# Performance work log

Hardware: AMD Instinct MI355X
Metric: run time of the kernel (lower is better)

The kernel has to match this reference:

```python
import jax, jax.numpy as jnp
import numpy as np
import math

B, T, LM, LD, LP, D = 32, 40, 24, 32, 16, 256
VM, VD, VP = 4000, 6000, 2000
LTOT = LM + LD + LP + 1


def _sdpa(q, k, v, scale=None):
    # softmax(q k^T [*scale]) v, over the last two dims (works for rank-3 and rank-4)
    a = jnp.matmul(q, jnp.swapaxes(k, -1, -2))
    if scale is not None:
        a = a * scale
    a = jax.nn.softmax(a, axis=-1)
    return jnp.matmul(a, v)


def _pos_table():
    # HiTANet-style sinusoidal table with a zero pad row at index 0
    pos = np.arange(T, dtype=np.float32)[:, None]
    j = np.arange(D)[None, :]
    ang = pos / np.power(10000.0, 2.0 * (j // 2) / float(D))
    pe = np.where(j % 2 == 0, np.sin(ang), np.cos(ang)).astype(np.float32)
    return jnp.asarray(np.concatenate([np.zeros((1, D), np.float32), pe], axis=0))


def setup_inputs():
    key = jax.random.key(0)
    ks = jax.random.split(key, 24)
    u = lambda k, shape, b: jax.random.uniform(k, shape, jnp.float32, -b, b)
    inp = {
        "med_codes": jax.random.randint(ks[0], (B, T, LM), 0, VM),
        "diag_codes": jax.random.randint(ks[1], (B, T, LD), 0, VD),
        "proc_codes": jax.random.randint(ks[2], (B, T, LP), 0, VP),
        "med_mask_code": (jax.random.uniform(ks[3], (B, T, LM, 1)) < 0.8).astype(jnp.float32),
        "diag_mask_code": (jax.random.uniform(ks[4], (B, T, LD, 1)) < 0.8).astype(jnp.float32),
        "proc_mask_code": (jax.random.uniform(ks[5], (B, T, LP, 1)) < 0.8).astype(jnp.float32),
        "seq_time_step": jax.random.uniform(ks[6], (B, T), jnp.float32) * 2.0,
        "input_len": jax.random.randint(ks[7], (B,), 1, T + 1),
        "emb_med": jax.random.normal(ks[8], (VM, D), jnp.float32) * 0.02,
        "emb_diag": jax.random.normal(ks[9], (VD, D), jnp.float32) * 0.02,
        "emb_proc": jax.random.normal(ks[10], (VP, D), jnp.float32) * 0.02,
        "bias_med": u(ks[11], (D,), 1.0 / math.sqrt(VM)),
        "W_sel": u(ks[12], (64, 1), 1.0),
        "b_sel": u(ks[13], (64,), 1.0),
        "W_time": u(ks[14], (D, 64), 1.0 / math.sqrt(64.0)),
        "b_time": u(ks[15], (D,), 1.0 / math.sqrt(64.0)),
        "Wg_med": u(ks[16], (D, D), 1.0 / math.sqrt(float(D))),
        "bg_med": u(ks[17], (D,), 1.0 / math.sqrt(float(D))),
        "Wg_diag": u(ks[18], (D, D), 1.0 / math.sqrt(float(D))),
        "bg_diag": u(ks[19], (D,), 1.0 / math.sqrt(float(D))),
        "Wg_proc": u(ks[20], (D, D), 1.0 / math.sqrt(float(D))),
        "bg_proc": u(ks[21], (D,), 1.0 / math.sqrt(float(D))),
        "hidden_size": 256,
    }
    return inp


def reference(med_codes, diag_codes, proc_codes, med_mask_code, diag_mask_code,
              proc_mask_code, seq_time_step, input_len, emb_med, emb_diag, emb_proc,
              bias_med, W_sel, b_sel, W_time, b_time, Wg_med, bg_med, Wg_diag,
              bg_diag, Wg_proc, bg_proc, hidden_size):
    scale = 1.0 / math.sqrt(hidden_size + 1e-7)

    # time encoding: W2(1 - tanh((W1 t + b1)^2)) + b2  -> [B,T,1,D]
    t = seq_time_step[:, :, None]                       # [B,T,1]
    tf = 1.0 - jnp.tanh((t @ W_sel.T + b_sel) ** 2)     # [B,T,64]
    tf = tf @ W_time.T + b_time                         # [B,T,D]
    time_feature = tf[:, :, None, :]                    # [B,T,1,D]

    # positional encoding: positions 1..len, 0 (pad row) beyond len
    pe = _pos_table()
    ar = jnp.arange(T)[None, :]
    pos_idx = jnp.where(ar < input_len[:, None], ar + 1, 0)
    output_pos = pe[pos_idx]                            # [B,T,D]

    # masked embedding gathers [B,T,L,D]
    out_med = emb_med[med_codes] * med_mask_code
    out_diag = emb_diag[diag_codes] * diag_mask_code
    out_proc = emb_proc[proc_codes] * proc_mask_code

    # time-gated sigmoid modulation
    def gate(out, Wg, bg):
        g = _sdpa(time_feature, out, out, scale)        # [B,T,1,D]
        g = jax.nn.sigmoid(g @ Wg.T + bg)
        return g * out                                  # broadcast over L

    out_med = gate(out_med, Wg_med, bg_med)
    out_diag = gate(out_diag, Wg_diag, bg_diag)
    out_proc = gate(out_proc, Wg_proc, bg_proc)

    # per-modality self-attention over flattened T*L tokens
    def visit_att(out, L):
        x = out.reshape(B, T * L, D)
        x = _sdpa(x, x, x, scale)
        return x.reshape(B, T, L, D)

    out_med = visit_att(out_med, LM)
    out_diag = visit_att(out_diag, LD)
    out_proc = visit_att(out_proc, LP)

    # concat-fusion self-attention over all code types + time token [B,T,LTOT,D]
    merge = jnp.concatenate([out_med, out_diag, out_proc, time_feature], axis=2)
    merge = _sdpa(merge, merge, merge, scale)

    # med branch (predDiag=False, predProc=False): re-concat of the splits == merge
    out_med = merge[:, :, :LM]
    merge_aux = merge.reshape(B * T, LTOT, D)
    med_trans = out_med.reshape(B * T, LM, D)
    med_att = _sdpa(med_trans, merge_aux, merge_aux)    # no scale (default None)
    out = med_att.sum(axis=1).reshape(B, T, D) + bias_med + output_pos
    return out  # dropout is identity at eval
```

## Files before the change

### kernel.cpp

```cpp
#include <hip/hip_runtime.h>
#include <hip/hip_bf16.h>
#include <math.h>

typedef float f32x4 __attribute__((ext_vector_type(4)));
typedef short s16x8 __attribute__((ext_vector_type(8)));
typedef unsigned short us;

__device__ __forceinline__ float bf2f(us u){
  union { unsigned int i; float f; } v; v.i = ((unsigned int)u) << 16; return v.f;
}
__device__ __forceinline__ us f2bf(float f){
  union { float f; unsigned int i; } v; v.f = f;
  unsigned int r = v.i + 0x7FFFu + ((v.i >> 16) & 1u);
  return (us)(r >> 16);
}
__device__ __forceinline__ float dot4(f32x4 a, f32x4 b){
  return a.x*b.x + a.y*b.y + a.z*b.z + a.w*b.w;
}
__device__ __forceinline__ f32x4 mfma16(s16x8 a, s16x8 b, f32x4 c){
  return __builtin_amdgcn_mfma_f32_16x16x32_bf16(a, b, c, 0, 0, 0);
}
__device__ __forceinline__ void gld16(const us* src, us* dst){
  __builtin_amdgcn_global_load_lds(
      (const __attribute__((address_space(1))) unsigned int*)src,
      (__attribute__((address_space(3))) unsigned int*)dst, 16, 0, 0);
}

__global__ __launch_bounds__(256) void tf_kernel(
    const float* __restrict__ seq, const float* __restrict__ Wsel,
    const float* __restrict__ bsel, const float* __restrict__ Wtime,
    const float* __restrict__ btime, float* __restrict__ tf)
{
  const int bt = blockIdx.x, tid = threadIdx.x;
  __shared__ float w1[64];
  float s = seq[bt];
  if (tid < 64){ float h = s*Wsel[tid] + bsel[tid]; w1[tid] = 1.0f - tanhf(h*h); }
  __syncthreads();
  const float* wrow = Wtime + (size_t)tid*64;
  float acc = btime[tid];
  #pragma unroll 8
  for (int j = 0; j < 64; ++j) acc += w1[j]*wrow[j];
  tf[(size_t)bt*256 + tid] = acc;
}

struct GateLds {
  float E[32*260];
  float sc[64];
  float tfs[256];
  float gs[256];
};

template<int L, int N>
__device__ __forceinline__ void gate_body(GateLds& S,
    const int* __restrict__ codes, const float* __restrict__ mask,
    const float* __restrict__ emb, const float* __restrict__ tf,
    const float* __restrict__ Wg, const float* __restrict__ bg,
    us* __restrict__ Xg, us* __restrict__ XgT, float scale, int bt)
{
  const int b = bt/40, t = bt - (bt/40)*40;
  const int tid = threadIdx.x, lane = tid & 63, wid = tid >> 6;

  S.tfs[tid] = tf[(size_t)bt*256 + tid];
  #pragma unroll
  for (int l = 0; l < L; ++l){
    int code = codes[bt*L + l];
    float m = mask[bt*L + l];
    S.E[l*260 + tid] = emb[(size_t)code*256 + tid] * m;
  }
  __syncthreads();

  constexpr int RPW = (L + 3)/4;
  #pragma unroll
  for (int rr = 0; rr < RPW; ++rr){
    int l = wid*RPW + rr;
    if (l < L){
      f32x4 e4 = *(const f32x4*)&S.E[l*260 + lane*4];
      f32x4 t4 = *(const f32x4*)&S.tfs[lane*4];
      float p = dot4(e4, t4);
      #pragma unroll
      for (int m = 1; m < 64; m <<= 1) p += __shfl_xor(p, m, 64);
      if (lane == 0) S.sc[l] = p * scale;
    }
  }
  __syncthreads();
  if (wid == 0){
    float p = (lane < L) ? __expf(S.sc[lane]) : 0.f;
    float ss = p;
    #pragma unroll
    for (int m = 1; m < 64; m <<= 1) ss += __shfl_xor(ss, m, 64);
    if (lane < L) S.sc[lane] = p / ss;
  }
  __syncthreads();

  float g = 0.f;
  #pragma unroll
  for (int l = 0; l < L; ++l) g += S.sc[l]*S.E[l*260 + tid];
  S.gs[tid] = g;
  __syncthreads();

  const float* wrow = Wg + (size_t)tid*256;
  float a2 = bg[tid];
  #pragma unroll
  for (int e = 0; e < 256; e += 4){
    f32x4 w4 = *(const f32x4*)&wrow[e];
    f32x4 g4 = *(const f32x4*)&S.gs[e];
    a2 += dot4(w4, g4);
  }
  float g2 = 1.f/(1.f + __expf(-a2));

  us tbuf[L];
  #pragma unroll
  for (int l = 0; l < L; ++l){
    us h = f2bf(g2 * S.E[l*260 + tid]);
    Xg[((size_t)b*N + t*L + l)*256 + tid] = h;
    tbuf[l] = h;
  }
  size_t tb = ((size_t)b*256 + tid)*N + (size_t)t*L;
  #pragma unroll
  for (int l = 0; l < L; l += 8){
    uint4 v;
    v.x = (unsigned)tbuf[l+0] | ((unsigned)tbuf[l+1] << 16);
    v.y = (unsigned)tbuf[l+2] | ((unsigned)tbuf[l+3] << 16);
    v.z = (unsigned)tbuf[l+4] | ((unsigned)tbuf[l+5] << 16);
    v.w = (unsigned)tbuf[l+6] | ((unsigned)tbuf[l+7] << 16);
    *(uint4*)&XgT[tb + l] = v;
  }
}

template<int L, int N>
__global__ __launch_bounds__(256) void gate_kernel(
    const int* codes, const float* mask, const float* emb, const float* tf,
    const float* Wg, const float* bg, us* Xg, us* XgT, float scale)
{
  __shared__ GateLds S;
  gate_body<L,N>(S, codes, mask, emb, tf, Wg, bg, Xg, XgT, scale, blockIdx.x);
}

__global__ __launch_bounds__(256) void gate_fused(
    const int* mc, const int* dc, const int* pc,
    const float* mm, const float* dm, const float* pm,
    const float* em, const float* ed, const float* ep,
    const float* tf,
    const float* Wgm, const float* bgm, const float* Wgd, const float* bgd,
    const float* Wgp, const float* bgp,
    us* Xm, us* XTm, us* Xd, us* XTd, us* Xp, us* XTp, float scale)
{
  __shared__ GateLds S;
  int bid = blockIdx.x;
  if (bid < 1280)      gate_body<24,960 >(S, mc, mm, em, tf, Wgm, bgm, Xm, XTm, scale, bid);
  else if (bid < 2560) gate_body<32,1280>(S, dc, dm, ed, tf, Wgd, bgd, Xd, XTd, scale, bid-1280);
  else                 gate_body<16,640 >(S, pc, pm, ep, tf, Wgp, bgp, Xp, XTp, scale, bid-2560);
}

struct VisitLds {
  us buf[33792];
  us ps[4*32*40];
};

__device__ __forceinline__ void stage_tile(VisitLds& S, int cur,
    const us* __restrict__ Xb, const us* __restrict__ XTb, int k0, int N_, int tid)
{
  const int wid = tid >> 6;
  us* KS = S.buf + cur*8192;
  us* VS = S.buf + 16384 + cur*8704;
  #pragma unroll
  for (int i = 0; i < 4; ++i){
    int c = tid + i*256;
    int row = c >> 5, ch = c & 31;
    gld16(Xb + (size_t)(k0 + row)*256 + (((ch*16) ^ ((row & 7) << 4)) >> 1),
          KS + (i*256 + wid*64)*8);
    int d = c >> 2, kslot = c & 3;
    gld16(XTb + (size_t)d*N_ + k0 + kslot*8,
          VS + (i*256 + wid*64)*8);
  }
}

template<int N>
__device__ __forceinline__ void visit_body(VisitLds& S,
    const us* __restrict__ Xb, const us* __restrict__ XTb,
    us* __restrict__ Outb, float scale, int q0)
{
  const int tid = threadIdx.x, lane = tid & 63, wid = tid >> 6;
  const int lc = lane & 15, lg = lane >> 4;

  #pragma unroll
  for (int i = 0; i < 16; ++i){
    int c = tid + i*256, row = c >> 5, ch = c & 31;
    int gr = q0 + row; gr = gr < N ? gr : N-1;
    gld16(Xb + (size_t)gr*256 + (((ch*16) ^ ((row & 7) << 4)) >> 1),
          S.buf + (i*256 + wid*64)*8);
  }
  __syncthreads();
  s16x8 qf[2][8];
  #pragma unroll
  for (int qg = 0; qg < 2; ++qg)
    #pragma unroll
    for (int kk = 0; kk < 8; ++kk){
      int row = wid*32 + qg*16 + lc;
      int off = kk*64 + lg*16;
      qf[qg][kk] = *(const s16x8*)((const char*)S.buf + row*512 + (off ^ ((row & 7) << 4)));
    }
  __syncthreads();

  if (tid < 512){
    us v = (tid < 32) ? (us)0x3F80 : (us)0;
    S.buf[16384 + 8192 + tid] = v;
    S.buf[25088 + 8192 + tid] = v;
  }
  stage_tile(S, 0, Xb, XTb, 0, N, tid);
  __syncthreads();

  f32x4 o[2][16];
  #pragma unroll
  for (int qg = 0; qg < 2; ++qg)
    #pragma unroll
    for (int dcc = 0; dcc < 16; ++dcc) o[qg][dcc] = (f32x4){0.f,0.f,0.f,0.f};
  f32x4 ls[2] = {(f32x4){0.f,0.f,0.f,0.f}, (f32x4){0.f,0.f,0.f,0.f}};

  us* pw = S.ps + wid*32*40;
  const int nt = N/32;
  int cur = 0;

  for (int t = 0; t < nt; ++t){
    if (t + 1 < nt) stage_tile(S, cur^1, Xb, XTb, (t+1)*32, N, tid);

    const us* KS = S.buf + cur*8192;
    const us* VS = S.buf + 16384 + cur*8704;

    f32x4 s[2][2];
    #pragma unroll
    for (int qg = 0; qg < 2; ++qg)
      #pragma unroll
      for (int kc = 0; kc < 2; ++kc) s[qg][kc] = (f32x4){0.f,0.f,0.f,0.f};
    #pragma unroll
    for (int kk = 0; kk < 8; ++kk){
      #pragma unroll
      for (int kc = 0; kc < 2; ++kc){
        int row = kc*16 + lc;
        int off = kk*64 + lg*16;
        s16x8 kb = *(const s16x8*)((const char*)KS + row*512 + (off ^ ((row & 7) << 4)));
        s[0][kc] = mfma16(qf[0][kk], kb, s[0][kc]);
        s[1][kc] = mfma16(qf[1][kk], kb, s[1][kc]);
      }
    }

    #pragma unroll
    for (int qg = 0; qg < 2; ++qg){
      #pragma unroll
      for (int r = 0; r < 4; ++r){
        float p0 = __expf(s[qg][0][r] * scale);
        float p1 = __expf(s[qg][1][r] * scale);
        int prow = qg*16 + lg*4 + r;
        pw[prow*40 + lc]      = f2bf(p0);
        pw[prow*40 + 16 + lc] = f2bf(p1);
      }
    }

    s16x8 pa[2];
    #pragma unroll
    for (int qg = 0; qg < 2; ++qg)
      pa[qg] = *(const s16x8*)(pw + (qg*16 + lc)*40 + lg*8);

    #pragma unroll
    for (int dcc = 0; dcc < 16; ++dcc){
      s16x8 vf = *(const s16x8*)(VS + (dcc*16 + lc)*32 + lg*8);
      o[0][dcc] = mfma16(pa[0], vf, o[0][dcc]);
      o[1][dcc] = mfma16(pa[1], vf, o[1][dcc]);
    }
    {
      s16x8 vf1 = *(const s16x8*)(VS + (256 + lc)*32 + lg*8);
      ls[0] = mfma16(pa[0], vf1, ls[0]);
      ls[1] = mfma16(pa[1], vf1, ls[1]);
    }

    __syncthreads();
    cur ^= 1;
  }

  #pragma unroll
  for (int qg = 0; qg < 2; ++qg){
    #pragma unroll
    for (int r = 0; r < 4; ++r){
      float lv = __shfl(ls[qg][r], lane & 48, 64);
      float inv = 1.f / lv;
      int grow = q0 + wid*32 + qg*16 + lg*4 + r;
      if (grow < N){
        #pragma unroll
        for (int dcc = 0; dcc < 16; ++dcc){
          Outb[(size_t)grow*256 + dcc*16 + lc] = f2bf(o[qg][dcc][r] * inv);
        }
      }
    }
  }
}

template<int N>
__global__ __launch_bounds__(256) void visit_kernel(
    const us* Xg, const us* XgT, us* Out, float scale)
{
  __shared__ VisitLds S;
  const int b = blockIdx.y;
  visit_body<N>(S, Xg + (size_t)b*N*256, XgT + (size_t)b*256*N,
                Out + (size_t)b*N*256, scale, blockIdx.x*128);
}

__global__ __launch_bounds__(256) void visit_fused(
    const us* Xm, const us* XTm, us* Am,
    const us* Xd, const us* XTd, us* Ad,
    const us* Xp, const us* XTp, us* Ap, float scale)
{
  __shared__ VisitLds S;
  int p = blockIdx.x;
  int l = (p & 7)*92 + (p >> 3);
  if (l < 256){
    int b = l >> 3, q0 = (l & 7)*128;
    visit_body<960>(S, Xm + (size_t)b*960*256, XTm + (size_t)b*256*960,
                    Am + (size_t)b*960*256, scale, q0);
  } else if (l < 576){
    int r = l - 256, b = r/10, q0 = (r - (r/10)*10)*128;
    visit_body<1280>(S, Xd + (size_t)b*1280*256, XTd + (size_t)b*256*1280,
                     Ad + (size_t)b*1280*256, scale, q0);
  } else {
    int r = l - 576, b = r/5, q0 = (r - (r/5)*5)*128;
    visit_body<640>(S, Xp + (size_t)b*640*256, XTp + (size_t)b*256*640,
                    Ap + (size_t)b*640*256, scale, q0);
  }
}

__global__ __launch_bounds__(512) void merge_kernel(
    const us* __restrict__ Amed, const us* __restrict__ Adiag,
    const us* __restrict__ Aproc, const float* __restrict__ tf,
    const float* __restrict__ bias, const int* __restrict__ ilen,
    float* __restrict__ out, float scale)
{
  __shared__ us Mb[80*256];
  __shared__ float Sr[80*84];
  __shared__ float P[80*84];
  __shared__ float W1[24*76];
  __shared__ float S2[24*76];
  __shared__ float wj[73];
  __shared__ float uk[73];

  const int bt = blockIdx.x, b = bt/40, t = bt - (bt/40)*40;
  const int tid = threadIdx.x, lane = tid & 63, wid = tid >> 6;
  const int lc = lane & 15, lg = lane >> 4;

  for (int c = tid; c < 72*32; c += 512){
    int row = c >> 5, ch = c & 31;
    const us* src;
    if (row < 24)      src = Amed  + ((size_t)b*960  + t*24 + row)*256      + ch*8;
    else if (row < 56) src = Adiag + ((size_t)b*1280 + t*32 + (row-24))*256 + ch*8;
    else               src = Aproc + ((size_t)b*640  + t*16 + (row-56))*256 + ch*8;
    uint4 v = *(const uint4*)src;
    *(uint4*)((char*)Mb + row*512 + ((ch*16) ^ ((row & 7) << 4))) = v;
  }
  if (tid < 256) Mb[72*256 + tid] = f2bf(tf[(size_t)bt*256 + tid]);
  for (int c = tid; c < 7*32; c += 512){
    int row = 73 + (c >> 5), ch = c & 31;
    *(uint4*)((char*)Mb + row*512 + ch*16) = (uint4){0,0,0,0};
  }
  __syncthreads();

  for (int tt = wid; tt < 25; tt += 8){
    int ti = tt/5, tj = tt - (tt/5)*5;
    f32x4 s = (f32x4){0.f,0.f,0.f,0.f};
    #pragma unroll
    for (int kk = 0; kk < 8; ++kk){
      int ra = ti*16 + lc, rb = tj*16 + lc;
      int off = kk*64 + lg*16;
      s16x8 a  = *(const s16x8*)((const char*)Mb + ra*512 + (off ^ ((ra & 7) << 4)));
      s16x8 bb = *(const s16x8*)((const char*)Mb + rb*512 + (off ^ ((rb & 7) << 4)));
      s = mfma16(a, bb, s);
    }
    #pragma unroll
    for (int r = 0; r < 4; ++r)
      Sr[(ti*16 + lg*4 + r)*84 + tj*16 + lc] = s[r];
  }
  __syncthreads();

  for (int r = wid; r < 73; r += 8){
    float e0 = __expf(scale * Sr[r*84 + lane]);
    float e1 = (lane < 9) ? __expf(scale * Sr[r*84 + 64 + lane]) : 0.f;
    float ss = e0 + e1;
    #pragma unroll
    for (int m = 1; m < 64; m <<= 1) ss += __shfl_xor(ss, m, 64);
    float inv = 1.f/ss;
    P[r*84 + lane] = e0 * inv;
    if (lane < 12) P[r*84 + 64 + lane] = (lane < 9) ? e1*inv : 0.f;
  }
  __syncthreads();

  if (tid < 456){
    int i = tid/19, mq = tid - (tid/19)*19;
    f32x4 acc = (f32x4){0.f,0.f,0.f,0.f};
    for (int k = 0; k < 73; ++k){
      float p = P[i*84 + k];
      f32x4 s4 = *(const f32x4*)&Sr[k*84 + mq*4];
      acc.x += p*s4.x; acc.y += p*s4.y; acc.z += p*s4.z; acc.w += p*s4.w;
    }
    *(f32x4*)&W1[i*76 + mq*4] = acc;
  }
  __syncthreads();

  for (int e = tid; e < 24*73; e += 512){
    int i = e/73, j = e - (e/73)*73;
    float acc = 0.f;
    #pragma unroll
    for (int mq = 0; mq < 19; ++mq)
      acc += dot4(*(const f32x4*)&W1[i*76 + mq*4], *(const f32x4*)&P[j*84 + mq*4]);
    S2[i*76 + j] = acc;
  }
  __syncthreads();

  for (int r = wid; r < 24; r += 8){
    float e0 = __expf(S2[r*76 + lane]);
    float e1 = (lane < 9) ? __expf(S2[r*76 + 64 + lane]) : 0.f;
    float ss = e0 + e1;
    #pragma unroll
    for (int m = 1; m < 64; m <<= 1) ss += __shfl_xor(ss, m, 64);
    float inv = 1.f/ss;
    S2[r*76 + lane] = e0*inv;
    if (lane < 12) S2[r*76 + 64 + lane] = (lane < 9) ? e1*inv : 0.f;
  }
  __syncthreads();

  if (tid < 73){
    float a = 0.f;
    #pragma unroll
    for (int i = 0; i < 24; ++i) a += S2[i*76 + tid];
    wj[tid] = a;
  }
  __syncthreads();
  if (tid < 73){
    float a = 0.f;
    for (int j = 0; j < 73; ++j) a += wj[j]*P[j*84 + tid];
    uk[tid] = a;
  }
  __syncthreads();

  if (tid < 256){
    float acc = bias[tid];
    if (t < ilen[b]){
      float ex = (float)(2*(tid>>1)) * (1.0f/256.0f);
      float dv = powf(10000.f, ex);
      float ang = (float)t / dv;
      acc += (tid & 1) ? cosf(ang) : sinf(ang);
    }
    for (int k = 0; k < 73; ++k){
      us m = *(const us*)((const char*)Mb + k*512 + ((tid*2) ^ ((k & 7) << 4)));
      acc += uk[k] * bf2f(m);
    }
    out[(size_t)bt*256 + tid] = acc;
  }
}

extern "C" void kernel_launch(void* const* d_in, const int* in_sizes, int n_in,
                              void* d_out, int out_size, void* d_ws, size_t ws_size,
                              hipStream_t stream)
{
  (void)in_sizes; (void)n_in; (void)out_size;

  const int*   med_codes = (const int*)  d_in[0];
  const int*   diag_codes= (const int*)  d_in[1];
  const int*   proc_codes= (const int*)  d_in[2];
  const float* med_mask  = (const float*)d_in[3];
  const float* diag_mask = (const float*)d_in[4];
  const float* proc_mask = (const float*)d_in[5];
  const float* seq_time  = (const float*)d_in[6];
  const int*   input_len = (const int*)  d_in[7];
  const float* emb_med   = (const float*)d_in[8];
  const float* emb_diag  = (const float*)d_in[9];
  const float* emb_proc  = (const float*)d_in[10];
  const float* bias_med  = (const float*)d_in[11];
  const float* W_sel     = (const float*)d_in[12];
  const float* b_sel     = (const float*)d_in[13];
  const float* W_time    = (const float*)d_in[14];
  const float* b_time    = (const float*)d_in[15];
  const float* Wg_med    = (const float*)d_in[16];
  const float* bg_med    = (const float*)d_in[17];
  const float* Wg_diag   = (const float*)d_in[18];
  const float* bg_diag   = (const float*)d_in[19];
  const float* Wg_proc   = (const float*)d_in[20];
  const float* bg_proc   = (const float*)d_in[21];

  const float scale = (float)(1.0 / sqrt(256.0 + 1e-7));

  char* ws = (char*)d_ws;
  const size_t sz_tf = (size_t)1280*256*4;
  const size_t szA_m = (size_t)32*960*256*2;
  const size_t szA_d = (size_t)32*1280*256*2;
  const size_t szA_p = (size_t)32*640*256*2;

  size_t off = 0;
  float* tf   = (float*)(ws + off); off += sz_tf;
  us* Am      = (us*)(ws + off);    off += szA_m;
  us* Ad      = (us*)(ws + off);    off += szA_d;
  us* Ap      = (us*)(ws + off);    off += szA_p;

  const size_t fused_need = off + 2*(szA_m + szA_d + szA_p);
  tf_kernel<<<1280, 256, 0, stream>>>(seq_time, W_sel, b_sel, W_time, b_time, tf);

  if (ws_size >= fused_need){
    us* Xm  = (us*)(ws + off); off += szA_m;
    us* XTm = (us*)(ws + off); off += szA_m;
    us* Xd  = (us*)(ws + off); off += szA_d;
    us* XTd = (us*)(ws + off); off += szA_d;
    us* Xp  = (us*)(ws + off); off += szA_p;
    us* XTp = (us*)(ws + off); off += szA_p;

    gate_fused<<<3840, 256, 0, stream>>>(
        med_codes, diag_codes, proc_codes, med_mask, diag_mask, proc_mask,
        emb_med, emb_diag, emb_proc, tf,
        Wg_med, bg_med, Wg_diag, bg_diag, Wg_proc, bg_proc,
        Xm, XTm, Xd, XTd, Xp, XTp, scale);

    visit_fused<<<736, 256, 0, stream>>>(Xm, XTm, Am, Xd, XTd, Ad, Xp, XTp, Ap, scale);
  } else {
    us* Xg  = (us*)(ws + off);
    us* XgT = (us*)(ws + off + szA_d);

    gate_kernel<24,960><<<1280, 256, 0, stream>>>(med_codes, med_mask, emb_med, tf, Wg_med, bg_med, Xg, XgT, scale);
    visit_kernel<960><<<dim3(8,32), 256, 0, stream>>>(Xg, XgT, Am, scale);

    gate_kernel<32,1280><<<1280, 256, 0, stream>>>(diag_codes, diag_mask, emb_diag, tf, Wg_diag, bg_diag, Xg, XgT, scale);
    visit_kernel<1280><<<dim3(10,32), 256, 0, stream>>>(Xg, XgT, Ad, scale);

    gate_kernel<16,640><<<1280, 256, 0, stream>>>(proc_codes, proc_mask, emb_proc, tf, Wg_proc, bg_proc, Xg, XgT, scale);
    visit_kernel<640><<<dim3(5,32), 256, 0, stream>>>(Xg, XgT, Ap, scale);
  }

  merge_kernel<<<1280, 512, 0, stream>>>(Am, Ad, Ap, tf, bias_med, input_len, (float*)d_out, scale);
}
```

Baseline: 442.6 us.

## Deepen visit-attention K/V prefetch, add MFMA priority, bf16 MFMA merge stages

The visit-attention body now loads Q fragments straight from global memory and stages two K/V tiles up front. The main loop uses explicit vmcnt/lgkmcnt waits and raw barriers so a tile two steps ahead is prefetched while the current one is computed, and s_setprio raises wave priority around the MFMA blocks. Launch bounds now request two blocks per CU. In the merge kernel, the fp32 scalar matmuls for P·S and W1·P become bf16 MFMA tiles with bf16 LDS buffers, which lowers LDS footprint and ALU work but adds bf16 rounding in the second attention score path.

```diff
diff --git a/kernel.cpp b/kernel.cpp
--- a/kernel.cpp
+++ b/kernel.cpp
@@ -25,6 +25,12 @@
       (const __attribute__((address_space(1))) unsigned int*)src,
       (__attribute__((address_space(3))) unsigned int*)dst, 16, 0, 0);
 }
+
+#define VM_WAIT8()  asm volatile("s_waitcnt vmcnt(8)" ::: "memory")
+#define VM_WAIT0()  asm volatile("s_waitcnt vmcnt(0)" ::: "memory")
+#define LGKM_WAIT0() asm volatile("s_waitcnt lgkmcnt(0)" ::: "memory")
+#define PRO_WAIT()  asm volatile("s_waitcnt vmcnt(8) lgkmcnt(0)" ::: "memory")
+#define BAR()       __builtin_amdgcn_s_barrier()
 
 __global__ __launch_bounds__(256) void tf_kernel(
     const float* __restrict__ seq, const float* __restrict__ Wsel,
@@ -183,32 +189,26 @@
   const int tid = threadIdx.x, lane = tid & 63, wid = tid >> 6;
   const int lc = lane & 15, lg = lane >> 4;
 
-  #pragma unroll
-  for (int i = 0; i < 16; ++i){
-    int c = tid + i*256, row = c >> 5, ch = c & 31;
-    int gr = q0 + row; gr = gr < N ? gr : N-1;
-    gld16(Xb + (size_t)gr*256 + (((ch*16) ^ ((row & 7) << 4)) >> 1),
-          S.buf + (i*256 + wid*64)*8);
-  }
-  __syncthreads();
   s16x8 qf[2][8];
   #pragma unroll
   for (int qg = 0; qg < 2; ++qg)
     #pragma unroll
     for (int kk = 0; kk < 8; ++kk){
-      int row = wid*32 + qg*16 + lc;
-      int off = kk*64 + lg*16;
-      qf[qg][kk] = *(const s16x8*)((const char*)S.buf + row*512 + (off ^ ((row & 7) << 4)));
-    }
-  __syncthreads();
-
-  if (tid < 512){
-    us v = (tid < 32) ? (us)0x3F80 : (us)0;
-    S.buf[16384 + 8192 + tid] = v;
-    S.buf[25088 + 8192 + tid] = v;
-  }
+      int gr = q0 + wid*32 + qg*16 + lc;
+      gr = gr < N ? gr : N-1;
+      qf[qg][kk] = *(const s16x8*)(Xb + (size_t)gr*256 + kk*32 + lg*8);
+    }
+
+  for (int i = tid; i < 512; i += 256){
+    us v = (i < 32) ? (us)0x3F80 : (us)0;
+    S.buf[16384 + 8192 + i] = v;
+    S.buf[25088 + 8192 + i] = v;
+  }
+
   stage_tile(S, 0, Xb, XTb, 0, N, tid);
-  __syncthreads();
+  stage_tile(S, 1, Xb, XTb, 32, N, tid);
+  PRO_WAIT();
+  BAR();
 
   f32x4 o[2][16];
   #pragma unroll
@@ -219,19 +219,18 @@
 
   us* pw = S.ps + wid*32*40;
   const int nt = N/32;
-  int cur = 0;
-
-  for (int t = 0; t < nt; ++t){
-    if (t + 1 < nt) stage_tile(S, cur^1, Xb, XTb, (t+1)*32, N, tid);
-
-    const us* KS = S.buf + cur*8192;
-    const us* VS = S.buf + 16384 + cur*8704;
+
+  auto compute_tile = [&](int c){
+    const us* KS = S.buf + c*8192;
+    const us* VS = S.buf + 16384 + c*8704;
 
     f32x4 s[2][2];
     #pragma unroll
     for (int qg = 0; qg < 2; ++qg)
       #pragma unroll
       for (int kc = 0; kc < 2; ++kc) s[qg][kc] = (f32x4){0.f,0.f,0.f,0.f};
+
+    __builtin_amdgcn_s_setprio(1);
     #pragma unroll
     for (int kk = 0; kk < 8; ++kk){
       #pragma unroll
@@ -243,6 +242,7 @@
         s[1][kc] = mfma16(qf[1][kk], kb, s[1][kc]);
       }
     }
+    __builtin_amdgcn_s_setprio(0);
 
     #pragma unroll
     for (int qg = 0; qg < 2; ++qg){
@@ -261,6 +261,7 @@
     for (int qg = 0; qg < 2; ++qg)
       pa[qg] = *(const s16x8*)(pw + (qg*16 + lc)*40 + lg*8);
 
+    __builtin_amdgcn_s_setprio(1);
     #pragma unroll
     for (int dcc = 0; dcc < 16; ++dcc){
       s16x8 vf = *(const s16x8*)(VS + (dcc*16 + lc)*32 + lg*8);
@@ -272,9 +273,21 @@
       ls[0] = mfma16(pa[0], vf1, ls[0]);
       ls[1] = mfma16(pa[1], vf1, ls[1]);
     }
-
-    __syncthreads();
-    cur ^= 1;
+    __builtin_amdgcn_s_setprio(0);
+  };
+
+  for (int t = 0; t < nt; ++t){
+    compute_tile(t & 1);
+    if (t == nt-1) break;
+    LGKM_WAIT0();
+    BAR();
+    if (t + 2 < nt){
+      stage_tile(S, t & 1, Xb, XTb, (t+2)*32, N, tid);
+      VM_WAIT8();
+    } else {
+      VM_WAIT0();
+    }
+    BAR();
   }
 
   #pragma unroll
@@ -295,7 +308,7 @@
 }
 
 template<int N>
-__global__ __launch_bounds__(256) void visit_kernel(
+__global__ __launch_bounds__(256, 2) void visit_kernel(
     const us* Xg, const us* XgT, us* Out, float scale)
 {
   __shared__ VisitLds S;
@@ -304,7 +317,7 @@
                 Out + (size_t)b*N*256, scale, blockIdx.x*128);
 }
 
-__global__ __launch_bounds__(256) void visit_fused(
+__global__ __launch_bounds__(256, 2) void visit_fused(
     const us* Xm, const us* XTm, us* Am,
     const us* Xd, const us* XTd, us* Ad,
     const us* Xp, const us* XTp, us* Ap, float scale)
@@ -327,19 +340,19 @@
   }
 }
 
-__global__ __launch_bounds__(512) void merge_kernel(
+__global__ __launch_bounds__(512, 2) void merge_kernel(
     const us* __restrict__ Amed, const us* __restrict__ Adiag,
     const us* __restrict__ Aproc, const float* __restrict__ tf,
     const float* __restrict__ bias, const int* __restrict__ ilen,
     float* __restrict__ out, float scale)
 {
-  __shared__ us Mb[80*256];
-  __shared__ float Sr[80*84];
-  __shared__ float P[80*84];
-  __shared__ float W1[24*76];
-  __shared__ float S2[24*76];
+  __shared__ alignas(16) us Mb[80*256];
+  __shared__ alignas(16) us SrB[80*96];
+  __shared__ alignas(16) us Pb[80*96];
+  __shared__ alignas(16) us W1B[32*96];
   __shared__ float wj[73];
   __shared__ float uk[73];
+  float* S2f = (float*)SrB;
 
   const int bt = blockIdx.x, b = bt/40, t = bt - (bt/40)*40;
   const int tid = threadIdx.x, lane = tid & 63, wid = tid >> 6;
@@ -374,66 +387,84 @@
     }
     #pragma unroll
     for (int r = 0; r < 4; ++r)
-      Sr[(ti*16 + lg*4 + r)*84 + tj*16 + lc] = s[r];
-  }
-  __syncthreads();
-
+      SrB[(ti*16 + lg*4 + r)*96 + tj*16 + lc] = f2bf(s[r]);
+  }
+  __syncthreads();
+
+  for (int c = tid; c < 80*16; c += 512){
+    int r = c >> 4;
+    SrB[r*96 + 80 + (c & 15)] = 0;
+  }
   for (int r = wid; r < 73; r += 8){
-    float e0 = __expf(scale * Sr[r*84 + lane]);
-    float e1 = (lane < 9) ? __expf(scale * Sr[r*84 + 64 + lane]) : 0.f;
+    float e0 = __expf(scale * bf2f(SrB[r*96 + lane]));
+    float e1 = (lane < 9) ? __expf(scale * bf2f(SrB[r*96 + 64 + lane])) : 0.f;
     float ss = e0 + e1;
     #pragma unroll
     for (int m = 1; m < 64; m <<= 1) ss += __shfl_xor(ss, m, 64);
     float inv = 1.f/ss;
-    P[r*84 + lane] = e0 * inv;
-    if (lane < 12) P[r*84 + 64 + lane] = (lane < 9) ? e1*inv : 0.f;
-  }
-  __syncthreads();
-
-  if (tid < 456){
-    int i = tid/19, mq = tid - (tid/19)*19;
-    f32x4 acc = (f32x4){0.f,0.f,0.f,0.f};
-    for (int k = 0; k < 73; ++k){
-      float p = P[i*84 + k];
-      f32x4 s4 = *(const f32x4*)&Sr[k*84 + mq*4];
-      acc.x += p*s4.x; acc.y += p*s4.y; acc.z += p*s4.z; acc.w += p*s4.w;
-    }
-    *(f32x4*)&W1[i*76 + mq*4] = acc;
-  }
-  __syncthreads();
-
-  for (int e = tid; e < 24*73; e += 512){
-    int i = e/73, j = e - (e/73)*73;
-    float acc = 0.f;
-    #pragma unroll
-    for (int mq = 0; mq < 19; ++mq)
-      acc += dot4(*(const f32x4*)&W1[i*76 + mq*4], *(const f32x4*)&P[j*84 + mq*4]);
-    S2[i*76 + j] = acc;
+    Pb[r*96 + lane] = f2bf(e0 * inv);
+    if (lane < 32) Pb[r*96 + 64 + lane] = (lane < 9) ? f2bf(e1*inv) : (us)0;
+  }
+  for (int c = tid; c < 7*96; c += 512){
+    Pb[73*96 + c] = 0;
+  }
+  __syncthreads();
+
+  for (int tt = wid; tt < 10; tt += 8){
+    int ri = tt/5, cj = tt - (tt/5)*5;
+    f32x4 s = (f32x4){0.f,0.f,0.f,0.f};
+    #pragma unroll
+    for (int kk = 0; kk < 3; ++kk){
+      s16x8 a  = *(const s16x8*)(Pb  + (ri*16 + lc)*96 + kk*32 + lg*8);
+      s16x8 bb = *(const s16x8*)(SrB + (cj*16 + lc)*96 + kk*32 + lg*8);
+      s = mfma16(a, bb, s);
+    }
+    #pragma unroll
+    for (int r = 0; r < 4; ++r)
+      W1B[(ri*16 + lg*4 + r)*96 + cj*16 + lc] = f2bf(s[r]);
+  }
+  if (tid < 512){
+    W1B[(tid >> 4)*96 + 80 + (tid & 15)] = 0;
+  }
+  __syncthreads();
+
+  for (int tt = wid; tt < 10; tt += 8){
+    int ri = tt/5, cj = tt - (tt/5)*5;
+    f32x4 s = (f32x4){0.f,0.f,0.f,0.f};
+    #pragma unroll
+    for (int kk = 0; kk < 3; ++kk){
+      s16x8 a  = *(const s16x8*)(W1B + (ri*16 + lc)*96 + kk*32 + lg*8);
+      s16x8 bb = *(const s16x8*)(Pb  + (cj*16 + lc)*96 + kk*32 + lg*8);
+      s = mfma16(a, bb, s);
+    }
+    #pragma unroll
+    for (int r = 0; r < 4; ++r)
+      S2f[(ri*16 + lg*4 + r)*84 + cj*16 + lc] = s[r];
   }
   __syncthreads();
 
   for (int r = wid; r < 24; r += 8){
-    float e0 = __expf(S2[r*76 + lane]);
-    float e1 = (lane < 9) ? __expf(S2[r*76 + 64 + lane]) : 0.f;
+    float e0 = __expf(S2f[r*84 + lane]);
+    float e1 = (lane < 9) ? __expf(S2f[r*84 + 64 + lane]) : 0.f;
     float ss = e0 + e1;
     #pragma unroll
     for (int m = 1; m < 64; m <<= 1) ss += __shfl_xor(ss, m, 64);
     float inv = 1.f/ss;
-    S2[r*76 + lane] = e0*inv;
-    if (lane < 12) S2[r*76 + 64 + lane] = (lane < 9) ? e1*inv : 0.f;
+    S2f[r*84 + lane] = e0*inv;
+    if (lane < 12) S2f[r*84 + 64 + lane] = (lane < 9) ? e1*inv : 0.f;
   }
   __syncthreads();
 
   if (tid < 73){
     float a = 0.f;
     #pragma unroll
-    for (int i = 0; i < 24; ++i) a += S2[i*76 + tid];
+    for (int i = 0; i < 24; ++i) a += S2f[i*84 + tid];
     wj[tid] = a;
   }
   __syncthreads();
   if (tid < 73){
     float a = 0.f;
-    for (int j = 0; j < 73; ++j) a += wj[j]*P[j*84 + tid];
+    for (int j = 0; j < 73; ++j) a += wj[j] * bf2f(Pb[j*96 + tid]);
     uk[tid] = a;
   }
   __syncthreads();
```

New measurement: 354.2 us. 1.25x faster.
